# Performance work log

Hardware: AMD Instinct MI355X
Metric: run time of the kernel (lower is better)

The kernel has to match this reference:

```python
import jax, jax.numpy as jnp
import numpy as np

B, H, N, C = 16, 64, 128, 256
HID = 1024   # feedforward hidden
C8 = C // 8  # mlp hidden in pos/score MLPs
EPS = 1e-6


def _ln(x, g, b):
    m = jnp.mean(x, axis=-1, keepdims=True)
    v = jnp.mean((x - m) ** 2, axis=-1, keepdims=True)
    return (x - m) / jnp.sqrt(v + EPS) * g + b


def setup_inputs() -> dict:
    key = jax.random.key(0)
    ks = jax.random.split(key, 24)
    s = lambda k, shape, scale=0.05: jax.random.normal(k, shape, dtype=jnp.float32) * scale
    inp = {
        "query_input": jax.random.normal(ks[0], (B, H, C), dtype=jnp.float32),
        "key_input": jax.random.normal(ks[1], (B, H, N, C), dtype=jnp.float32),
        "relative_pos": jax.random.normal(ks[2], (B, H, N, 4), dtype=jnp.float32),
        "visibility_mask": jax.random.randint(ks[3], (B, H, N, 1), 0, 2, dtype=jnp.int32),
        # layernorms
        "ln1_g": jnp.ones((C,), jnp.float32), "ln1_b": jnp.zeros((C,), jnp.float32),
        "ln2_g": jnp.ones((C,), jnp.float32), "ln2_b": jnp.zeros((C,), jnp.float32),
        # attention projections (no bias)
        "Wq": s(ks[4], (C, C)), "Wk": s(ks[5], (C, C)), "Wv": s(ks[6], (C, C)),
        # position MLP: 4 -> C//8 -> C
        "pos_w1": s(ks[7], (4, C8)), "pos_b1": jnp.zeros((C8,), jnp.float32),
        "pos_w2": s(ks[8], (C8, C)), "pos_b2": jnp.zeros((C,), jnp.float32),
        # score MLP: C -> C//8 -> C
        "sc_w1": s(ks[9], (C, C8)), "sc_b1": jnp.zeros((C8,), jnp.float32),
        "sc_w2": s(ks[10], (C8, C)), "sc_b2": jnp.zeros((C,), jnp.float32),
        # output layer
        "Wo": s(ks[11], (C, C)), "bo": jnp.zeros((C,), jnp.float32),
        # feedforward MLP: C -> HID -> C
        "ff_w1": s(ks[12], (C, HID)), "ff_b1": jnp.zeros((HID,), jnp.float32),
        "ff_w2": s(ks[13], (HID, C)), "ff_b2": jnp.zeros((C,), jnp.float32),
    }
    return inp


def reference(query_input, key_input, relative_pos, visibility_mask,
              ln1_g, ln1_b, ln2_g, ln2_b, Wq, Wk, Wv,
              pos_w1, pos_b1, pos_w2, pos_b2,
              sc_w1, sc_b1, sc_w2, sc_b2, Wo, bo,
              ff_w1, ff_b1, ff_w2, ff_b2):
    # --- attention block with pre-norm + residual ---
    x = _ln(query_input, ln1_g, ln1_b)                      # [B,H,C]
    q = x @ Wq                                              # [B,H,C]
    k = key_input @ Wk                                      # [B,H,N,C]
    v = key_input @ Wv                                      # [B,H,N,C]
    pos = jax.nn.relu(relative_pos @ pos_w1 + pos_b1) @ pos_w2 + pos_b2  # [B,H,N,C]
    attn_in = k - q[:, :, None, :] + pos                    # [B,H,N,C]
    aw = jax.nn.relu(attn_in @ sc_w1 + sc_b1) @ sc_w2 + sc_b2  # [B,H,N,C]
    aw = jnp.where(visibility_mask == 0, -1e9, aw)
    aw = jax.nn.softmax(aw, axis=-2)                        # softmax over N
    agg = jnp.sum((v + pos) * aw, axis=2)                   # [B,H,C]
    attn_out = agg @ Wo + bo
    x = attn_out + query_input
    # --- feedforward block with pre-norm + residual ---
    y = _ln(x, ln2_g, ln2_b)
    y = jax.nn.relu(y @ ff_w1 + ff_b1) @ ff_w2 + ff_b2
    return y + x
```

## Files before the change

### kernel.cpp

```cpp
#include <hip/hip_runtime.h>
#include <math.h>

#define NN 128
#define CC 256
#define HIDN 1024
#define KST 264
#define SST 40
#define EPSL 1e-6f

typedef short s16x8 __attribute__((ext_vector_type(8)));
typedef float f32x4 __attribute__((ext_vector_type(4)));

#define WVOFF    0
#define WTOFF    73728
#define SW2OFF   82944
#define WOB_OFF  91136
#define FW1B_OFF 156672
#define FW2B_OFF 418816
#define QT_BYTE_OFF   1361920
#define AGG_BYTE_OFF  1492992
#define WQT_BYTE_OFF  2541568
#define QTC_BYTE_OFF  2574336

__device__ __forceinline__ unsigned short f2b(float x) {
    unsigned u = __builtin_bit_cast(unsigned, x);
    u += 0x7fffu + ((u >> 16) & 1u);
    return (unsigned short)(u >> 16);
}
__device__ __forceinline__ float b2f(unsigned short s) {
    return __builtin_bit_cast(float, ((unsigned)s) << 16);
}
__device__ __forceinline__ float blo(unsigned u) { return b2f((unsigned short)u); }
__device__ __forceinline__ float bhi(unsigned u) { return b2f((unsigned short)(u >> 16)); }
__device__ __forceinline__ unsigned pack2(float a, float b) {
    return (unsigned)f2b(a) | ((unsigned)f2b(b) << 16);
}

__device__ __forceinline__ float block_sum_256(float v, float* red) {
    #pragma unroll
    for (int off = 32; off > 0; off >>= 1)
        v += __shfl_down(v, off, 64);
    const int wid = threadIdx.x >> 6;
    if ((threadIdx.x & 63) == 0) red[wid] = v;
    __syncthreads();
    float s = red[0] + red[1] + red[2] + red[3];
    __syncthreads();
    return s;
}

__global__ __launch_bounds__(256)
void prep_all(const float* __restrict__ Wk, const float* __restrict__ Wv,
              const float* __restrict__ Wq,
              const float* __restrict__ pw2, const float* __restrict__ sw1,
              const float* __restrict__ sw2, const float* __restrict__ fw1,
              const float* __restrict__ fw2, const float* __restrict__ Wo,
              const float* __restrict__ pb2, const float* __restrict__ sb1,
              unsigned short* __restrict__ ws16,
              float* __restrict__ wqt, float* __restrict__ qtc)
{
    int e = blockIdx.x * 256 + threadIdx.x;
    unsigned short v[8];
    if (e < 9216) {
        int koct = e >> 8, col = e & 255;
        #pragma unroll
        for (int j = 0; j < 8; ++j) {
            int k = koct * 8 + j;
            float val = (k < 256) ? Wv[k * 256 + col] : pw2[(k - 256) * 256 + col];
            v[j] = f2b(val);
        }
        int dest = WVOFF + (col >> 4) * 4608 + (koct >> 2) * 512
                 + (((((koct & 3) << 4) | (col & 15))) << 3);
        uint4 pk;
        pk.x = (unsigned)v[0] | ((unsigned)v[1] << 16);
        pk.y = (unsigned)v[2] | ((unsigned)v[3] << 16);
        pk.z = (unsigned)v[4] | ((unsigned)v[5] << 16);
        pk.w = (unsigned)v[6] | ((unsigned)v[7] << 16);
        *(uint4*)&ws16[dest] = pk;
    } else if (e < 10240) {
        int i = e - 9216;
        int koct = i & 3, col = i >> 2;
        #pragma unroll
        for (int j = 0; j < 8; ++j) v[j] = f2b(sw2[(koct * 8 + j) * 256 + col]);
        int dest = SW2OFF + (col >> 4) * 512 + ((((koct << 4) | (col & 15))) << 3);
        uint4 pk;
        pk.x = (unsigned)v[0] | ((unsigned)v[1] << 16);
        pk.y = (unsigned)v[2] | ((unsigned)v[3] << 16);
        pk.z = (unsigned)v[4] | ((unsigned)v[5] << 16);
        pk.w = (unsigned)v[6] | ((unsigned)v[7] << 16);
        *(uint4*)&ws16[dest] = pk;
    } else if (e < 83968) {
        const float* src; int base, i;
        if (e < 43008)      { src = fw1; base = FW1B_OFF; i = (e - 10240) * 8; }
        else if (e < 75776) { src = fw2; base = FW2B_OFF; i = (e - 43008) * 8; }
        else                { src = Wo;  base = WOB_OFF;  i = (e - 75776) * 8; }
        float4 a = *(const float4*)(src + i);
        float4 b = *(const float4*)(src + i + 4);
        uint4 pk;
        pk.x = pack2(a.x, a.y);
        pk.y = pack2(a.z, a.w);
        pk.z = pack2(b.x, b.y);
        pk.w = pack2(b.z, b.w);
        *(uint4*)&ws16[base + i] = pk;
    } else if (e < 93184) {
        int tid = e - 83968;
        int k = tid >> 5, j = tid & 31;
        const float* row = (k < 256) ? (Wk + (size_t)k * 256) : (pw2 + (size_t)(k - 256) * 256);
        float s = 0.0f;
        for (int c = 0; c < 256; ++c) s = fmaf(row[c], sw1[c * 32 + j], s);
        int dest = WTOFF + ((j >> 4) * 9 + (k >> 5)) * 512
                 + ((((((k >> 3) & 3) << 4) | (j & 15))) << 3) + (k & 7);
        ws16[dest] = f2b(s);
    } else if (e < 101376) {
        int tid = e - 93184;
        int c = tid >> 5, j = tid & 31;
        const float* row = Wq + (size_t)c * 256;
        float s = 0.0f;
        for (int cp = 0; cp < 256; ++cp) s = fmaf(row[cp], sw1[cp * 32 + j], s);
        wqt[c * 32 + j] = s;
    } else {
        int j = e - 101376;
        if (j < 32) {
            float s = sb1[j];
            for (int c = 0; c < 256; ++c) s = fmaf(pb2[c], sw1[c * 32 + j], s);
            qtc[j] = s;
        }
    }
}

__global__ __launch_bounds__(256)
void qprep2(const float* __restrict__ qin,
            const float* __restrict__ ln1g, const float* __restrict__ ln1b,
            const float* __restrict__ wqt, const float* __restrict__ qtc,
            float* __restrict__ qt)
{
    __shared__ __align__(16) float xlnL[4][CC];
    const int t = threadIdx.x;
    const int lane = t & 63;
    const int r = t >> 6;
    const int b0 = blockIdx.x * 4;
    const size_t rowoff = (size_t)(b0 + r) * CC;

    float v0 = qin[rowoff + lane];
    float v1 = qin[rowoff + lane + 64];
    float v2 = qin[rowoff + lane + 128];
    float v3 = qin[rowoff + lane + 192];
    float s = v0 + v1 + v2 + v3;
    #pragma unroll
    for (int off = 32; off > 0; off >>= 1) s += __shfl_xor(s, off);
    float mean = s * (1.0f / CC);
    float d0 = v0 - mean, d1 = v1 - mean, d2 = v2 - mean, d3 = v3 - mean;
    float vs = d0 * d0 + d1 * d1 + d2 * d2 + d3 * d3;
    #pragma unroll
    for (int off = 32; off > 0; off >>= 1) vs += __shfl_xor(vs, off);
    float rstd = rsqrtf(vs * (1.0f / CC) + EPSL);
    xlnL[r][lane]       = d0 * rstd * ln1g[lane] + ln1b[lane];
    xlnL[r][lane + 64]  = d1 * rstd * ln1g[lane + 64] + ln1b[lane + 64];
    xlnL[r][lane + 128] = d2 * rstd * ln1g[lane + 128] + ln1b[lane + 128];
    xlnL[r][lane + 192] = d3 * rstd * ln1g[lane + 192] + ln1b[lane + 192];
    __syncthreads();

    if (t < 128) {
        int r2 = t >> 5, j = t & 31;
        float acc = qtc[j];
        for (int c = 0; c < 256; ++c) acc = fmaf(-xlnL[r2][c], wqt[c * 32 + j], acc);
        qt[(size_t)(b0 + r2) * 32 + j] = acc;
    }
}

__global__ __launch_bounds__(256, 2)
void cft_attn(const float* __restrict__ kin, const float* __restrict__ rel,
              const int* __restrict__ vis,
              const float* __restrict__ pw1, const float* __restrict__ pb1,
              const float* __restrict__ pb2, const float* __restrict__ sb2,
              const unsigned short* __restrict__ ws16,
              const float* __restrict__ qt,
              float* __restrict__ aggout)
{
    __shared__ __align__(16) unsigned char smem[80032];
    unsigned short* keyb = (unsigned short*)smem;
    float* poolA = (float*)(smem + 77824);
    float* poolB = (float*)(smem + 78848);
    unsigned char* visb = smem + 79872;
    float* aggpool = (float*)smem;
    float* lpool   = (float*)(smem + 4096);

    const int bh = blockIdx.x;
    const int t = threadIdx.x;
    const int lane = t & 63;
    const int wvid = t >> 6;
    const int quad = lane >> 4;
    const int l16 = lane & 15;
    const int rb = wvid * 32;
    unsigned short* strip = (unsigned short*)(smem + 67584) + wvid * (32 * SST);

    const float4* kb4 = (const float4*)(kin + (size_t)bh * NN * CC);
    #pragma unroll
    for (int i = 0; i < 32; ++i) {
        int flat = i * 256 + t;
        int row = flat >> 6;
        int cu = flat & 63;
        float4 kv = kb4[flat];
        uint2 pk;
        pk.x = pack2(kv.x, kv.y);
        pk.y = pack2(kv.z, kv.w);
        *(uint2*)&keyb[row * KST + cu * 4] = pk;
    }
    if (t < NN) visb[t] = (unsigned char)(vis[(size_t)bh * NN + t] != 0);
    poolB[t] = pb2[t];

    union { s16x8 v; unsigned short u[8]; } phf0, phf1;
    {
        const int row0 = rb + l16, row1 = rb + 16 + l16;
        float4 r40 = *(const float4*)(rel + ((size_t)bh * NN + row0) * 4);
        float4 r41 = *(const float4*)(rel + ((size_t)bh * NN + row1) * 4);
        #pragma unroll
        for (int j = 0; j < 8; ++j) {
            int col = quad * 8 + j;
            float w0 = pw1[col], w1 = pw1[32 + col], w2 = pw1[64 + col], w3 = pw1[96 + col];
            float b = pb1[col];
            float v0 = fmaf(r40.x, w0, fmaf(r40.y, w1, fmaf(r40.z, w2, fmaf(r40.w, w3, b))));
            float v1 = fmaf(r41.x, w0, fmaf(r41.y, w1, fmaf(r41.z, w2, fmaf(r41.w, w3, b))));
            phf0.u[j] = f2b(fmaxf(v0, 0.0f));
            phf1.u[j] = f2b(fmaxf(v1, 0.0f));
        }
    }
    const float qt0 = qt[(size_t)bh * 32 + l16];
    const float qt1 = qt[(size_t)bh * 32 + 16 + l16];
    __syncthreads();

    const int aoff0 = (rb + l16) * KST;
    const int aoff1 = (rb + 16 + l16) * KST;
    const unsigned short* wsv = ws16 + WVOFF;
    const unsigned short* wst = ws16 + WTOFF;
    const unsigned short* ws2 = ws16 + SW2OFF;

    unsigned char vm[2][4];
    #pragma unroll
    for (int mt = 0; mt < 2; ++mt)
        #pragma unroll
        for (int r = 0; r < 4; ++r) vm[mt][r] = visb[rb + mt * 16 + quad * 4 + r];

    f32x4 hacc[2][2];
    #pragma unroll
    for (int mt = 0; mt < 2; ++mt)
        #pragma unroll
        for (int jt = 0; jt < 2; ++jt) hacc[mt][jt] = (f32x4){0.f, 0.f, 0.f, 0.f};
    #pragma unroll
    for (int kt = 0; kt < 8; ++kt) {
        s16x8 A0 = *(const s16x8*)&keyb[aoff0 + kt * 32 + quad * 8];
        s16x8 A1 = *(const s16x8*)&keyb[aoff1 + kt * 32 + quad * 8];
        #pragma unroll
        for (int jt = 0; jt < 2; ++jt) {
            s16x8 B = *(const s16x8*)(wst + (size_t)(jt * 9 + kt) * 512 + lane * 8);
            hacc[0][jt] = __builtin_amdgcn_mfma_f32_16x16x32_bf16(A0, B, hacc[0][jt], 0, 0, 0);
            hacc[1][jt] = __builtin_amdgcn_mfma_f32_16x16x32_bf16(A1, B, hacc[1][jt], 0, 0, 0);
        }
    }
    #pragma unroll
    for (int jt = 0; jt < 2; ++jt) {
        s16x8 B = *(const s16x8*)(wst + (size_t)(jt * 9 + 8) * 512 + lane * 8);
        hacc[0][jt] = __builtin_amdgcn_mfma_f32_16x16x32_bf16(phf0.v, B, hacc[0][jt], 0, 0, 0);
        hacc[1][jt] = __builtin_amdgcn_mfma_f32_16x16x32_bf16(phf1.v, B, hacc[1][jt], 0, 0, 0);
    }
    #pragma unroll
    for (int mt = 0; mt < 2; ++mt)
        #pragma unroll
        for (int jt = 0; jt < 2; ++jt) {
            float qv = jt ? qt1 : qt0;
            int rw = (mt * 16 + quad * 4) * SST + jt * 16 + l16;
            strip[rw]           = f2b(fmaxf(hacc[mt][jt][0] + qv, 0.0f));
            strip[rw + SST]     = f2b(fmaxf(hacc[mt][jt][1] + qv, 0.0f));
            strip[rw + 2 * SST] = f2b(fmaxf(hacc[mt][jt][2] + qv, 0.0f));
            strip[rw + 3 * SST] = f2b(fmaxf(hacc[mt][jt][3] + qv, 0.0f));
        }

    s16x8 H0 = *(const s16x8*)&strip[l16 * SST + quad * 8];
    s16x8 H1 = *(const s16x8*)&strip[(16 + l16) * SST + quad * 8];
    float mloc[16];
    #pragma unroll
    for (int ct = 0; ct < 16; ++ct) {
        f32x4 a0 = (f32x4){0.f, 0.f, 0.f, 0.f};
        f32x4 a1 = (f32x4){0.f, 0.f, 0.f, 0.f};
        s16x8 B = *(const s16x8*)(ws2 + ((size_t)ct * 64 + lane) * 8);
        a0 = __builtin_amdgcn_mfma_f32_16x16x32_bf16(H0, B, a0, 0, 0, 0);
        a1 = __builtin_amdgcn_mfma_f32_16x16x32_bf16(H1, B, a1, 0, 0, 0);
        float sb2c = sb2[ct * 16 + l16];
        float ml = -3.0e38f;
        #pragma unroll
        for (int r = 0; r < 4; ++r) {
            float s0 = vm[0][r] ? (a0[r] + sb2c) : -1e9f;
            float s1 = vm[1][r] ? (a1[r] + sb2c) : -1e9f;
            ml = fmaxf(ml, fmaxf(s0, s1));
        }
        ml = fmaxf(ml, __shfl_xor(ml, 16));
        ml = fmaxf(ml, __shfl_xor(ml, 32));
        mloc[ct] = ml;
    }
    __syncthreads();
    #pragma unroll 1
    for (int w = 0; w < 4; ++w) {
        if (wvid == w && lane < 16) {
            #pragma unroll
            for (int ct = 0; ct < 16; ++ct) {
                int x = ct * 16 + lane;
                poolA[x] = (w == 0) ? mloc[ct] : fmaxf(poolA[x], mloc[ct]);
            }
        }
        __syncthreads();
    }
    float Mf[16];
    #pragma unroll
    for (int ct = 0; ct < 16; ++ct) Mf[ct] = poolA[ct * 16 + l16];

    float lsp[16], aggp[16];
    #pragma unroll
    for (int ct = 0; ct < 16; ++ct) { lsp[ct] = 0.0f; aggp[ct] = 0.0f; }

    #pragma unroll 1
    for (int ck = 0; ck < 8; ++ck) {
        float ev[2][2][4];
        #pragma unroll
        for (int ctl = 0; ctl < 2; ++ctl) {
            int ct = ck * 2 + ctl;
            f32x4 a0 = (f32x4){0.f, 0.f, 0.f, 0.f};
            f32x4 a1 = (f32x4){0.f, 0.f, 0.f, 0.f};
            s16x8 B = *(const s16x8*)(ws2 + ((size_t)ct * 64 + lane) * 8);
            a0 = __builtin_amdgcn_mfma_f32_16x16x32_bf16(H0, B, a0, 0, 0, 0);
            a1 = __builtin_amdgcn_mfma_f32_16x16x32_bf16(H1, B, a1, 0, 0, 0);
            float sb2c = sb2[ct * 16 + l16];
            float M = Mf[ct];
            float ls = 0.0f;
            #pragma unroll
            for (int r = 0; r < 4; ++r) {
                float s0 = vm[0][r] ? (a0[r] + sb2c) : -1e9f;
                float s1 = vm[1][r] ? (a1[r] + sb2c) : -1e9f;
                float e0 = __expf(s0 - M);
                float e1 = __expf(s1 - M);
                ev[ctl][0][r] = e0;
                ev[ctl][1][r] = e1;
                ls += e0 + e1;
            }
            lsp[ct] = ls;
        }
        f32x4 acc[2][2];
        #pragma unroll
        for (int mt = 0; mt < 2; ++mt)
            #pragma unroll
            for (int ctl = 0; ctl < 2; ++ctl) acc[mt][ctl] = (f32x4){0.f, 0.f, 0.f, 0.f};
        #pragma unroll
        for (int kt = 0; kt < 8; ++kt) {
            s16x8 A0 = *(const s16x8*)&keyb[aoff0 + kt * 32 + quad * 8];
            s16x8 A1 = *(const s16x8*)&keyb[aoff1 + kt * 32 + quad * 8];
            #pragma unroll
            for (int ctl = 0; ctl < 2; ++ctl) {
                s16x8 B = *(const s16x8*)(wsv + ((size_t)((ck * 2 + ctl) * 9 + kt) * 512) + lane * 8);
                acc[0][ctl] = __builtin_amdgcn_mfma_f32_16x16x32_bf16(A0, B, acc[0][ctl], 0, 0, 0);
                acc[1][ctl] = __builtin_amdgcn_mfma_f32_16x16x32_bf16(A1, B, acc[1][ctl], 0, 0, 0);
            }
        }
        #pragma unroll
        for (int ctl = 0; ctl < 2; ++ctl) {
            s16x8 B = *(const s16x8*)(wsv + ((size_t)((ck * 2 + ctl) * 9 + 8) * 512) + lane * 8);
            acc[0][ctl] = __builtin_amdgcn_mfma_f32_16x16x32_bf16(phf0.v, B, acc[0][ctl], 0, 0, 0);
            acc[1][ctl] = __builtin_amdgcn_mfma_f32_16x16x32_bf16(phf1.v, B, acc[1][ctl], 0, 0, 0);
        }
        #pragma unroll
        for (int ctl = 0; ctl < 2; ++ctl) {
            const int ct = ck * 2 + ctl;
            float pb = poolB[ct * 16 + l16];
            float a = aggp[ct];
            #pragma unroll
            for (int mt = 0; mt < 2; ++mt)
                #pragma unroll
                for (int r = 0; r < 4; ++r)
                    a = fmaf(ev[ctl][mt][r], acc[mt][ctl][r] + pb, a);
            aggp[ct] = a;
        }
    }

    __syncthreads();
    #pragma unroll
    for (int ct = 0; ct < 16; ++ct) {
        float a = aggp[ct];
        a += __shfl_xor(a, 16);
        a += __shfl_xor(a, 32);
        float l = lsp[ct];
        l += __shfl_xor(l, 16);
        l += __shfl_xor(l, 32);
        if (lane < 16) {
            aggpool[wvid * 256 + ct * 16 + lane] = a;
            lpool[wvid * 256 + ct * 16 + lane] = l;
        }
    }
    __syncthreads();
    {
        float asum = aggpool[t] + aggpool[256 + t] + aggpool[512 + t] + aggpool[768 + t];
        float lsum = lpool[t] + lpool[256 + t] + lpool[512 + t] + lpool[768 + t];
        aggout[(size_t)bh * CC + t] = asum / lsum;
    }
}

__global__ __launch_bounds__(256, 4)
void cft_ffo2(const float* __restrict__ aggp, const float* __restrict__ qin,
              const float* __restrict__ bo,
              const float* __restrict__ ln2g, const float* __restrict__ ln2b,
              const unsigned short* __restrict__ ws16,
              const float* __restrict__ fb1, const float* __restrict__ fb2,
              float* __restrict__ out)
{
    __shared__ __align__(16) float aggL[2][CC];
    __shared__ __align__(16) float xlnL[2][CC];
    __shared__ __align__(16) float ffh[2][HIDN];
    __shared__ __align__(16) float part[2][2][CC];
    __shared__ float red[4];
    const int t = threadIdx.x;
    const int b0 = blockIdx.x * 2;
    const unsigned short* wob  = ws16 + WOB_OFF;
    const unsigned short* fw1b = ws16 + FW1B_OFF;
    const unsigned short* fw2b = ws16 + FW2B_OFF;

    float xq[2];
    #pragma unroll
    for (int i = 0; i < 2; ++i) {
        aggL[i][t] = aggp[(size_t)(b0 + i) * CC + t];
        xq[i] = qin[(size_t)(b0 + i) * CC + t];
    }
    __syncthreads();

    float ao[2];
    { float b = bo[t]; ao[0] = b; ao[1] = b; }
    for (int k4 = 0; k4 < CC / 4; ++k4) {
        float4 a0 = *(const float4*)&aggL[0][k4 * 4];
        float4 a1 = *(const float4*)&aggL[1][k4 * 4];
        const unsigned short* w = wob + (size_t)(k4 * 4) * CC + t;
        float w0 = b2f(w[0]), w1 = b2f(w[CC]), w2 = b2f(w[2 * CC]), w3 = b2f(w[3 * CC]);
        ao[0] = fmaf(a0.x, w0, fmaf(a0.y, w1, fmaf(a0.z, w2, fmaf(a0.w, w3, ao[0]))));
        ao[1] = fmaf(a1.x, w0, fmaf(a1.y, w1, fmaf(a1.z, w2, fmaf(a1.w, w3, ao[1]))));
    }
    float xrs[2] = { ao[0] + xq[0], ao[1] + xq[1] };

    #pragma unroll
    for (int row = 0; row < 2; ++row) {
        float x = xrs[row];
        float mean = block_sum_256(x, red) * (1.0f / CC);
        float d = x - mean;
        float var = block_sum_256(d * d, red) * (1.0f / CC);
        xlnL[row][t] = d * rsqrtf(var + EPSL) * ln2g[t] + ln2b[t];
    }
    __syncthreads();

    {
        const int h0 = 2 * t;
        float acc[2][4];
        acc[0][0] = acc[1][0] = fb1[h0];
        acc[0][1] = acc[1][1] = fb1[h0 + 1];
        acc[0][2] = acc[1][2] = fb1[h0 + 512];
        acc[0][3] = acc[1][3] = fb1[h0 + 513];
        for (int k4 = 0; k4 < CC / 4; ++k4) {
            float4 x0 = *(const float4*)&xlnL[0][k4 * 4];
            float4 x1 = *(const float4*)&xlnL[1][k4 * 4];
            float xa0[4] = {x0.x, x0.y, x0.z, x0.w};
            float xa1[4] = {x1.x, x1.y, x1.z, x1.w};
            #pragma unroll
            for (int kk = 0; kk < 4; ++kk) {
                const int k = k4 * 4 + kk;
                unsigned wA = *(const unsigned*)&fw1b[(size_t)k * HIDN + h0];
                unsigned wB = *(const unsigned*)&fw1b[(size_t)k * HIDN + h0 + 512];
                float wl = blo(wA), wh = bhi(wA), wl2 = blo(wB), wh2 = bhi(wB);
                acc[0][0] = fmaf(xa0[kk], wl, acc[0][0]);
                acc[0][1] = fmaf(xa0[kk], wh, acc[0][1]);
                acc[0][2] = fmaf(xa0[kk], wl2, acc[0][2]);
                acc[0][3] = fmaf(xa0[kk], wh2, acc[0][3]);
                acc[1][0] = fmaf(xa1[kk], wl, acc[1][0]);
                acc[1][1] = fmaf(xa1[kk], wh, acc[1][1]);
                acc[1][2] = fmaf(xa1[kk], wl2, acc[1][2]);
                acc[1][3] = fmaf(xa1[kk], wh2, acc[1][3]);
            }
        }
        #pragma unroll
        for (int row = 0; row < 2; ++row) {
            ffh[row][h0]       = fmaxf(acc[row][0], 0.0f);
            ffh[row][h0 + 1]   = fmaxf(acc[row][1], 0.0f);
            ffh[row][h0 + 512] = fmaxf(acc[row][2], 0.0f);
            ffh[row][h0 + 513] = fmaxf(acc[row][3], 0.0f);
        }
    }
    __syncthreads();

    {
        const int u = t & 127;
        const int half = t >> 7;
        const int c0 = 2 * u;
        const int hbase = half * 512;
        float oacc[2][2] = {{0.f, 0.f}, {0.f, 0.f}};
        for (int h4 = 0; h4 < 128; ++h4) {
            const int h = hbase + h4 * 4;
            #pragma unroll
            for (int hh = 0; hh < 4; ++hh) {
                unsigned w = *(const unsigned*)&fw2b[(size_t)(h + hh) * CC + c0];
                float w0 = blo(w), w1 = bhi(w);
                float hv0 = ffh[0][h + hh];
                float hv1 = ffh[1][h + hh];
                oacc[0][0] = fmaf(hv0, w0, oacc[0][0]);
                oacc[0][1] = fmaf(hv0, w1, oacc[0][1]);
                oacc[1][0] = fmaf(hv1, w0, oacc[1][0]);
                oacc[1][1] = fmaf(hv1, w1, oacc[1][1]);
            }
        }
        part[half][0][c0]     = oacc[0][0];
        part[half][0][c0 + 1] = oacc[0][1];
        part[half][1][c0]     = oacc[1][0];
        part[half][1][c0 + 1] = oacc[1][1];
    }
    __syncthreads();
    #pragma unroll
    for (int row = 0; row < 2; ++row)
        out[(size_t)(b0 + row) * CC + t] =
            xrs[row] + fb2[t] + part[0][row][t] + part[1][row][t];
}

extern "C" void kernel_launch(void* const* d_in, const int* in_sizes, int n_in,
                              void* d_out, int out_size, void* d_ws, size_t ws_size,
                              hipStream_t stream) {
    const float* qin  = (const float*)d_in[0];
    const float* kin  = (const float*)d_in[1];
    const float* rel  = (const float*)d_in[2];
    const int*   vis  = (const int*)  d_in[3];
    const float* ln1g = (const float*)d_in[4];
    const float* ln1b = (const float*)d_in[5];
    const float* ln2g = (const float*)d_in[6];
    const float* ln2b = (const float*)d_in[7];
    const float* Wq   = (const float*)d_in[8];
    const float* Wk   = (const float*)d_in[9];
    const float* Wv   = (const float*)d_in[10];
    const float* pw1  = (const float*)d_in[11];
    const float* pb1  = (const float*)d_in[12];
    const float* pw2  = (const float*)d_in[13];
    const float* pb2  = (const float*)d_in[14];
    const float* sw1  = (const float*)d_in[15];
    const float* sb1  = (const float*)d_in[16];
    const float* sw2  = (const float*)d_in[17];
    const float* sb2  = (const float*)d_in[18];
    const float* Wo   = (const float*)d_in[19];
    const float* bo   = (const float*)d_in[20];
    const float* fw1  = (const float*)d_in[21];
    const float* fb1  = (const float*)d_in[22];
    const float* fw2  = (const float*)d_in[23];
    const float* fb2  = (const float*)d_in[24];
    (void)in_sizes; (void)n_in; (void)out_size; (void)ws_size;

    unsigned short* ws16 = (unsigned short*)d_ws;
    float* qt   = (float*)((char*)d_ws + QT_BYTE_OFF);
    float* aggb = (float*)((char*)d_ws + AGG_BYTE_OFF);
    float* wqt  = (float*)((char*)d_ws + WQT_BYTE_OFF);
    float* qtc  = (float*)((char*)d_ws + QTC_BYTE_OFF);
    float* o = (float*)d_out;

    prep_all<<<dim3(397), dim3(256), 0, stream>>>(
        Wk, Wv, Wq, pw2, sw1, sw2, fw1, fw2, Wo, pb2, sb1, ws16, wqt, qtc);
    qprep2<<<dim3(256), dim3(256), 0, stream>>>(qin, ln1g, ln1b, wqt, qtc, qt);
    cft_attn<<<dim3(1024), dim3(256), 0, stream>>>(
        kin, rel, vis, pw1, pb1, pb2, sb2, ws16, qt, aggb);
    cft_ffo2<<<dim3(512), dim3(256), 0, stream>>>(
        aggb, qin, bo, ln2g, ln2b, ws16, fb1, fb2, o);
}
```

Before: 350.0 us.

## Split attention kernel work by output columns per wave with swizzled LDS

New measurement: 333.8 us. -4.6%, faster.

```diff
diff --git a/kernel.cpp b/kernel.cpp
--- a/kernel.cpp
+++ b/kernel.cpp
@@ -176,13 +176,9 @@
               const float* __restrict__ qt,
               float* __restrict__ aggout)
 {
-    __shared__ __align__(16) unsigned char smem[80032];
+    __shared__ __align__(16) unsigned char smem[81920];
     unsigned short* keyb = (unsigned short*)smem;
-    float* poolA = (float*)(smem + 77824);
-    float* poolB = (float*)(smem + 78848);
-    unsigned char* visb = smem + 79872;
-    float* aggpool = (float*)smem;
-    float* lpool   = (float*)(smem + 4096);
+    unsigned short* aux  = (unsigned short*)(smem + 65536);
 
     const int bh = blockIdx.x;
     const int t = threadIdx.x;
@@ -190,8 +186,7 @@
     const int wvid = t >> 6;
     const int quad = lane >> 4;
     const int l16 = lane & 15;
-    const int rb = wvid * 32;
-    unsigned short* strip = (unsigned short*)(smem + 67584) + wvid * (32 * SST);
+    const int rb_w = wvid * 32;
 
     const float4* kb4 = (const float4*)(kin + (size_t)bh * NN * CC);
     #pragma unroll
@@ -203,16 +198,17 @@
         uint2 pk;
         pk.x = pack2(kv.x, kv.y);
         pk.y = pack2(kv.z, kv.w);
-        *(uint2*)&keyb[row * KST + cu * 4] = pk;
-    }
-    if (t < NN) visb[t] = (unsigned char)(vis[(size_t)bh * NN + t] != 0);
-    poolB[t] = pb2[t];
+        int us = row * 256 + ((((cu >> 1) ^ (row & 7)) << 3) | ((cu & 1) << 2));
+        *(uint2*)&keyb[us] = pk;
+    }
+    const unsigned long long vm0 = __ballot(vis[(size_t)bh * NN + lane] != 0);
+    const unsigned long long vm1 = __ballot(vis[(size_t)bh * NN + 64 + lane] != 0);
 
     union { s16x8 v; unsigned short u[8]; } phf0, phf1;
+    const int prow0 = rb_w + l16, prow1 = rb_w + 16 + l16;
     {
-        const int row0 = rb + l16, row1 = rb + 16 + l16;
-        float4 r40 = *(const float4*)(rel + ((size_t)bh * NN + row0) * 4);
-        float4 r41 = *(const float4*)(rel + ((size_t)bh * NN + row1) * 4);
+        float4 r40 = *(const float4*)(rel + ((size_t)bh * NN + prow0) * 4);
+        float4 r41 = *(const float4*)(rel + ((size_t)bh * NN + prow1) * 4);
         #pragma unroll
         for (int j = 0; j < 8; ++j) {
             int col = quad * 8 + j;
@@ -223,180 +219,144 @@
             phf0.u[j] = f2b(fmaxf(v0, 0.0f));
             phf1.u[j] = f2b(fmaxf(v1, 0.0f));
         }
+        *(s16x8*)&aux[prow0 * 64 + (((4 + quad) ^ (prow0 & 7)) << 3)] = phf0.v;
+        *(s16x8*)&aux[prow1 * 64 + (((4 + quad) ^ (prow1 & 7)) << 3)] = phf1.v;
     }
     const float qt0 = qt[(size_t)bh * 32 + l16];
     const float qt1 = qt[(size_t)bh * 32 + 16 + l16];
     __syncthreads();
 
-    const int aoff0 = (rb + l16) * KST;
-    const int aoff1 = (rb + 16 + l16) * KST;
+    {
+        const unsigned short* wst = ws16 + WTOFF;
+        const int r0 = rb_w + l16;
+        const int r1 = rb_w + 16 + l16;
+        const int sw0 = r0 & 7;
+        f32x4 hacc[2][2];
+        #pragma unroll
+        for (int mt = 0; mt < 2; ++mt)
+            #pragma unroll
+            for (int jt = 0; jt < 2; ++jt) hacc[mt][jt] = (f32x4){0.f, 0.f, 0.f, 0.f};
+        #pragma unroll
+        for (int kt = 0; kt < 8; ++kt) {
+            s16x8 A0 = *(const s16x8*)&keyb[r0 * 256 + (((kt * 4 + quad) ^ sw0) << 3)];
+            s16x8 A1 = *(const s16x8*)&keyb[r1 * 256 + (((kt * 4 + quad) ^ sw0) << 3)];
+            #pragma unroll
+            for (int jt = 0; jt < 2; ++jt) {
+                s16x8 B = *(const s16x8*)(wst + (size_t)(jt * 9 + kt) * 512 + lane * 8);
+                hacc[0][jt] = __builtin_amdgcn_mfma_f32_16x16x32_bf16(A0, B, hacc[0][jt], 0, 0, 0);
+                hacc[1][jt] = __builtin_amdgcn_mfma_f32_16x16x32_bf16(A1, B, hacc[1][jt], 0, 0, 0);
+            }
+        }
+        #pragma unroll
+        for (int jt = 0; jt < 2; ++jt) {
+            s16x8 B = *(const s16x8*)(wst + (size_t)(jt * 9 + 8) * 512 + lane * 8);
+            hacc[0][jt] = __builtin_amdgcn_mfma_f32_16x16x32_bf16(phf0.v, B, hacc[0][jt], 0, 0, 0);
+            hacc[1][jt] = __builtin_amdgcn_mfma_f32_16x16x32_bf16(phf1.v, B, hacc[1][jt], 0, 0, 0);
+        }
+        #pragma unroll
+        for (int mt = 0; mt < 2; ++mt)
+            #pragma unroll
+            for (int jt = 0; jt < 2; ++jt) {
+                float qv = jt ? qt1 : qt0;
+                #pragma unroll
+                for (int r = 0; r < 4; ++r) {
+                    int n = rb_w + mt * 16 + quad * 4 + r;
+                    int col = jt * 16 + l16;
+                    aux[n * 64 + (((col >> 3) ^ (n & 7)) << 3) + (col & 7)] =
+                        f2b(fmaxf(hacc[mt][jt][r] + qv, 0.0f));
+                }
+            }
+    }
+    __syncthreads();
+
     const unsigned short* wsv = ws16 + WVOFF;
-    const unsigned short* wst = ws16 + WTOFF;
     const unsigned short* ws2 = ws16 + SW2OFF;
 
-    unsigned char vm[2][4];
-    #pragma unroll
-    for (int mt = 0; mt < 2; ++mt)
-        #pragma unroll
-        for (int r = 0; r < 4; ++r) vm[mt][r] = visb[rb + mt * 16 + quad * 4 + r];
-
-    f32x4 hacc[2][2];
-    #pragma unroll
-    for (int mt = 0; mt < 2; ++mt)
-        #pragma unroll
-        for (int jt = 0; jt < 2; ++jt) hacc[mt][jt] = (f32x4){0.f, 0.f, 0.f, 0.f};
-    #pragma unroll
-    for (int kt = 0; kt < 8; ++kt) {
-        s16x8 A0 = *(const s16x8*)&keyb[aoff0 + kt * 32 + quad * 8];
-        s16x8 A1 = *(const s16x8*)&keyb[aoff1 + kt * 32 + quad * 8];
-        #pragma unroll
-        for (int jt = 0; jt < 2; ++jt) {
-            s16x8 B = *(const s16x8*)(wst + (size_t)(jt * 9 + kt) * 512 + lane * 8);
-            hacc[0][jt] = __builtin_amdgcn_mfma_f32_16x16x32_bf16(A0, B, hacc[0][jt], 0, 0, 0);
-            hacc[1][jt] = __builtin_amdgcn_mfma_f32_16x16x32_bf16(A1, B, hacc[1][jt], 0, 0, 0);
-        }
-    }
-    #pragma unroll
-    for (int jt = 0; jt < 2; ++jt) {
-        s16x8 B = *(const s16x8*)(wst + (size_t)(jt * 9 + 8) * 512 + lane * 8);
-        hacc[0][jt] = __builtin_amdgcn_mfma_f32_16x16x32_bf16(phf0.v, B, hacc[0][jt], 0, 0, 0);
-        hacc[1][jt] = __builtin_amdgcn_mfma_f32_16x16x32_bf16(phf1.v, B, hacc[1][jt], 0, 0, 0);
-    }
-    #pragma unroll
-    for (int mt = 0; mt < 2; ++mt)
-        #pragma unroll
-        for (int jt = 0; jt < 2; ++jt) {
-            float qv = jt ? qt1 : qt0;
-            int rw = (mt * 16 + quad * 4) * SST + jt * 16 + l16;
-            strip[rw]           = f2b(fmaxf(hacc[mt][jt][0] + qv, 0.0f));
-            strip[rw + SST]     = f2b(fmaxf(hacc[mt][jt][1] + qv, 0.0f));
-            strip[rw + 2 * SST] = f2b(fmaxf(hacc[mt][jt][2] + qv, 0.0f));
-            strip[rw + 3 * SST] = f2b(fmaxf(hacc[mt][jt][3] + qv, 0.0f));
-        }
-
-    s16x8 H0 = *(const s16x8*)&strip[l16 * SST + quad * 8];
-    s16x8 H1 = *(const s16x8*)&strip[(16 + l16) * SST + quad * 8];
-    float mloc[16];
-    #pragma unroll
-    for (int ct = 0; ct < 16; ++ct) {
-        f32x4 a0 = (f32x4){0.f, 0.f, 0.f, 0.f};
-        f32x4 a1 = (f32x4){0.f, 0.f, 0.f, 0.f};
-        s16x8 B = *(const s16x8*)(ws2 + ((size_t)ct * 64 + lane) * 8);
-        a0 = __builtin_amdgcn_mfma_f32_16x16x32_bf16(H0, B, a0, 0, 0, 0);
-        a1 = __builtin_amdgcn_mfma_f32_16x16x32_bf16(H1, B, a1, 0, 0, 0);
-        float sb2c = sb2[ct * 16 + l16];
-        float ml = -3.0e38f;
-        #pragma unroll
-        for (int r = 0; r < 4; ++r) {
-            float s0 = vm[0][r] ? (a0[r] + sb2c) : -1e9f;
-            float s1 = vm[1][r] ? (a1[r] + sb2c) : -1e9f;
-            ml = fmaxf(ml, fmaxf(s0, s1));
-        }
-        ml = fmaxf(ml, __shfl_xor(ml, 16));
-        ml = fmaxf(ml, __shfl_xor(ml, 32));
-        mloc[ct] = ml;
-    }
-    __syncthreads();
     #pragma unroll 1
-    for (int w = 0; w < 4; ++w) {
-        if (wvid == w && lane < 16) {
-            #pragma unroll
-            for (int ct = 0; ct < 16; ++ct) {
-                int x = ct * 16 + lane;
-                poolA[x] = (w == 0) ? mloc[ct] : fmaxf(poolA[x], mloc[ct]);
-            }
-        }
-        __syncthreads();
-    }
-    float Mf[16];
-    #pragma unroll
-    for (int ct = 0; ct < 16; ++ct) Mf[ct] = poolA[ct * 16 + l16];
-
-    float lsp[16], aggp[16];
-    #pragma unroll
-    for (int ct = 0; ct < 16; ++ct) { lsp[ct] = 0.0f; aggp[ct] = 0.0f; }
-
-    #pragma unroll 1
-    for (int ck = 0; ck < 8; ++ck) {
-        float ev[2][2][4];
-        #pragma unroll
-        for (int ctl = 0; ctl < 2; ++ctl) {
-            int ct = ck * 2 + ctl;
+    for (int ck = 0; ck < 2; ++ck) {
+        const int ct0 = wvid * 4 + ck * 2;
+        s16x8 Bs0 = *(const s16x8*)(ws2 + ((size_t)ct0 * 64 + lane) * 8);
+        s16x8 Bs1 = *(const s16x8*)(ws2 + ((size_t)(ct0 + 1) * 64 + lane) * 8);
+        const float sb2c0 = sb2[ct0 * 16 + l16];
+        const float sb2c1 = sb2[(ct0 + 1) * 16 + l16];
+
+        float ml0 = -3.0e38f, ml1 = -3.0e38f;
+        #pragma unroll
+        for (int rb = 0; rb < 8; ++rb) {
+            const int n0 = rb * 16 + l16;
+            s16x8 H = *(const s16x8*)&aux[n0 * 64 + ((quad ^ (n0 & 7)) << 3)];
             f32x4 a0 = (f32x4){0.f, 0.f, 0.f, 0.f};
             f32x4 a1 = (f32x4){0.f, 0.f, 0.f, 0.f};
-            s16x8 B = *(const s16x8*)(ws2 + ((size_t)ct * 64 + lane) * 8);
-            a0 = __builtin_amdgcn_mfma_f32_16x16x32_bf16(H0, B, a0, 0, 0, 0);
-            a1 = __builtin_amdgcn_mfma_f32_16x16x32_bf16(H1, B, a1, 0, 0, 0);
-            float sb2c = sb2[ct * 16 + l16];
-            float M = Mf[ct];
-            float ls = 0.0f;
+            a0 = __builtin_amdgcn_mfma_f32_16x16x32_bf16(H, Bs0, a0, 0, 0, 0);
+            a1 = __builtin_amdgcn_mfma_f32_16x16x32_bf16(H, Bs1, a1, 0, 0, 0);
+            const unsigned long long m = (rb < 4) ? vm0 : vm1;
+            const int nb = (rb * 16) & 63;
             #pragma unroll
             for (int r = 0; r < 4; ++r) {
-                float s0 = vm[0][r] ? (a0[r] + sb2c) : -1e9f;
-                float s1 = vm[1][r] ? (a1[r] + sb2c) : -1e9f;
-                float e0 = __expf(s0 - M);
-                float e1 = __expf(s1 - M);
-                ev[ctl][0][r] = e0;
-                ev[ctl][1][r] = e1;
-                ls += e0 + e1;
-            }
-            lsp[ct] = ls;
-        }
-        f32x4 acc[2][2];
-        #pragma unroll
-        for (int mt = 0; mt < 2; ++mt)
-            #pragma unroll
-            for (int ctl = 0; ctl < 2; ++ctl) acc[mt][ctl] = (f32x4){0.f, 0.f, 0.f, 0.f};
-        #pragma unroll
-        for (int kt = 0; kt < 8; ++kt) {
-            s16x8 A0 = *(const s16x8*)&keyb[aoff0 + kt * 32 + quad * 8];
-            s16x8 A1 = *(const s16x8*)&keyb[aoff1 + kt * 32 + quad * 8];
-            #pragma unroll
-            for (int ctl = 0; ctl < 2; ++ctl) {
-                s16x8 B = *(const s16x8*)(wsv + ((size_t)((ck * 2 + ctl) * 9 + kt) * 512) + lane * 8);
-                acc[0][ctl] = __builtin_amdgcn_mfma_f32_16x16x32_bf16(A0, B, acc[0][ctl], 0, 0, 0);
-                acc[1][ctl] = __builtin_amdgcn_mfma_f32_16x16x32_bf16(A1, B, acc[1][ctl], 0, 0, 0);
-            }
-        }
-        #pragma unroll
-        for (int ctl = 0; ctl < 2; ++ctl) {
-            s16x8 B = *(const s16x8*)(wsv + ((size_t)((ck * 2 + ctl) * 9 + 8) * 512) + lane * 8);
-            acc[0][ctl] = __builtin_amdgcn_mfma_f32_16x16x32_bf16(phf0.v, B, acc[0][ctl], 0, 0, 0);
-            acc[1][ctl] = __builtin_amdgcn_mfma_f32_16x16x32_bf16(phf1.v, B, acc[1][ctl], 0, 0, 0);
-        }
-        #pragma unroll
-        for (int ctl = 0; ctl < 2; ++ctl) {
-            const int ct = ck * 2 + ctl;
-            float pb = poolB[ct * 16 + l16];
-            float a = aggp[ct];
-            #pragma unroll
-            for (int mt = 0; mt < 2; ++mt)
-                #pragma unroll
-                for (int r = 0; r < 4; ++r)
-                    a = fmaf(ev[ctl][mt][r], acc[mt][ctl][r] + pb, a);
-            aggp[ct] = a;
-        }
-    }
-
-    __syncthreads();
-    #pragma unroll
-    for (int ct = 0; ct < 16; ++ct) {
-        float a = aggp[ct];
-        a += __shfl_xor(a, 16);
-        a += __shfl_xor(a, 32);
-        float l = lsp[ct];
-        l += __shfl_xor(l, 16);
-        l += __shfl_xor(l, 32);
+                bool vv = (m >> (nb + quad * 4 + r)) & 1;
+                float s0 = vv ? (a0[r] + sb2c0) : -1e9f;
+                float s1 = vv ? (a1[r] + sb2c1) : -1e9f;
+                ml0 = fmaxf(ml0, s0);
+                ml1 = fmaxf(ml1, s1);
+            }
+        }
+        ml0 = fmaxf(ml0, __shfl_xor(ml0, 16)); ml0 = fmaxf(ml0, __shfl_xor(ml0, 32));
+        ml1 = fmaxf(ml1, __shfl_xor(ml1, 16)); ml1 = fmaxf(ml1, __shfl_xor(ml1, 32));
+
+        s16x8 Bv0[9], Bv1[9];
+        #pragma unroll
+        for (int kt = 0; kt < 9; ++kt) {
+            Bv0[kt] = *(const s16x8*)(wsv + (size_t)(ct0 * 9 + kt) * 512 + lane * 8);
+            Bv1[kt] = *(const s16x8*)(wsv + (size_t)((ct0 + 1) * 9 + kt) * 512 + lane * 8);
+        }
+        const float pbv0 = pb2[ct0 * 16 + l16];
+        const float pbv1 = pb2[(ct0 + 1) * 16 + l16];
+
+        float agg0 = 0.f, agg1 = 0.f, ls0 = 0.f, ls1 = 0.f;
+        #pragma unroll 2
+        for (int rb = 0; rb < 8; ++rb) {
+            const int n0 = rb * 16 + l16;
+            const int sw0 = n0 & 7;
+            const unsigned short* arow = &keyb[n0 * 256];
+            s16x8 H  = *(const s16x8*)&aux[n0 * 64 + ((quad ^ sw0) << 3)];
+            s16x8 PH = *(const s16x8*)&aux[n0 * 64 + (((4 + quad) ^ sw0) << 3)];
+            f32x4 a0 = (f32x4){0.f, 0.f, 0.f, 0.f};
+            f32x4 a1 = (f32x4){0.f, 0.f, 0.f, 0.f};
+            a0 = __builtin_amdgcn_mfma_f32_16x16x32_bf16(H, Bs0, a0, 0, 0, 0);
+            a1 = __builtin_amdgcn_mfma_f32_16x16x32_bf16(H, Bs1, a1, 0, 0, 0);
+            f32x4 v0a = (f32x4){0.f, 0.f, 0.f, 0.f};
+            f32x4 v1a = (f32x4){0.f, 0.f, 0.f, 0.f};
+            #pragma unroll
+            for (int kt = 0; kt < 8; ++kt) {
+                s16x8 A = *(const s16x8*)&arow[(((kt * 4 + quad) ^ sw0) << 3)];
+                v0a = __builtin_amdgcn_mfma_f32_16x16x32_bf16(A, Bv0[kt], v0a, 0, 0, 0);
+                v1a = __builtin_amdgcn_mfma_f32_16x16x32_bf16(A, Bv1[kt], v1a, 0, 0, 0);
+            }
+            v0a = __builtin_amdgcn_mfma_f32_16x16x32_bf16(PH, Bv0[8], v0a, 0, 0, 0);
+            v1a = __builtin_amdgcn_mfma_f32_16x16x32_bf16(PH, Bv1[8], v1a, 0, 0, 0);
+            const unsigned long long m = (rb < 4) ? vm0 : vm1;
+            const int nb = (rb * 16) & 63;
+            #pragma unroll
+            for (int r = 0; r < 4; ++r) {
+                bool vv = (m >> (nb + quad * 4 + r)) & 1;
+                float sc0 = vv ? (a0[r] + sb2c0) : -1e9f;
+                float sc1 = vv ? (a1[r] + sb2c1) : -1e9f;
+                float e0 = __expf(sc0 - ml0);
+                float e1 = __expf(sc1 - ml1);
+                ls0 += e0;
+                ls1 += e1;
+                agg0 = fmaf(e0, v0a[r] + pbv0, agg0);
+                agg1 = fmaf(e1, v1a[r] + pbv1, agg1);
+            }
+        }
+        agg0 += __shfl_xor(agg0, 16); agg0 += __shfl_xor(agg0, 32);
+        ls0  += __shfl_xor(ls0, 16);  ls0  += __shfl_xor(ls0, 32);
+        agg1 += __shfl_xor(agg1, 16); agg1 += __shfl_xor(agg1, 32);
+        ls1  += __shfl_xor(ls1, 16);  ls1  += __shfl_xor(ls1, 32);
         if (lane < 16) {
-            aggpool[wvid * 256 + ct * 16 + lane] = a;
-            lpool[wvid * 256 + ct * 16 + lane] = l;
-        }
-    }
-    __syncthreads();
-    {
-        float asum = aggpool[t] + aggpool[256 + t] + aggpool[512 + t] + aggpool[768 + t];
-        float lsum = lpool[t] + lpool[256 + t] + lpool[512 + t] + lpool[768 + t];
-        aggout[(size_t)bh * CC + t] = asum / lsum;
+            aggout[(size_t)bh * CC + ct0 * 16 + l16]       = agg0 / ls0;
+            aggout[(size_t)bh * CC + (ct0 + 1) * 16 + l16] = agg1 / ls1;
+        }
     }
 }
 
```
